# Kernel tuning notes

Hardware: AMD Instinct MI355X
Metric: run time of the kernel (lower is better)

Reference implementation:

```python
import jax, jax.numpy as jnp
import numpy as np

N = 50000      # nodes
E = 625000     # directed edges
F_IN, H1, H2, OUT = 128, 128, 64, 50


def setup_inputs() -> dict:
    key = jax.random.key(0)
    ks = jax.random.split(key, 5)
    x = jax.random.normal(ks[0], (N, F_IN), dtype=jnp.float32)
    edge_index = jax.random.randint(ks[1], (2, E), 0, N, dtype=jnp.int64)
    W1 = jax.random.normal(ks[2], (F_IN, H1), dtype=jnp.float32) * 0.05
    b1 = jnp.zeros((H1,), jnp.float32)
    W2 = jax.random.normal(ks[3], (H1, H2), dtype=jnp.float32) * 0.05
    b2 = jnp.zeros((H2,), jnp.float32)
    Wh = jax.random.normal(ks[4], (H2, OUT), dtype=jnp.float32) * 0.05
    bh = jnp.zeros((OUT,), jnp.float32)
    return {"x": x, "edge_index": edge_index, "W1": W1, "b1": b1,
            "W2": W2, "b2": b2, "Wh": Wh, "bh": bh}


def _gcn_conv(h, W, b, src, dst, dinv, n):
    # h' = D^{-1/2} A_hat D^{-1/2} (h W) + b, A_hat includes self-loops
    h = h @ W                                   # [n, out]
    coef = (dinv[src] * dinv[dst])[:, None]      # [e, 1]
    agg = jax.ops.segment_sum(h[src] * coef, dst, num_segments=n)
    return agg + b


def reference(x, edge_index, W1, b1, W2, b2, Wh, bh):
    n = x.shape[0]
    loops = jnp.arange(n, dtype=edge_index.dtype)
    src = jnp.concatenate([edge_index[0], loops])
    dst = jnp.concatenate([edge_index[1], loops])
    # symmetric GCN normalization: deg over destinations (incl. self-loops)
    deg = jax.ops.segment_sum(jnp.ones(src.shape[0], x.dtype), dst, num_segments=n)
    dinv = jnp.where(deg > 0, jax.lax.rsqrt(deg), 0.0)
    # dropout is a no-op in eval mode (training=False)
    h = _gcn_conv(x, W1, b1, src, dst, dinv, n)
    h = jax.nn.relu(h)
    h = _gcn_conv(h, W2, b2, src, dst, dinv, n)
    h = jax.nn.relu(h)
    return h @ Wh + bh
```

## Files before the change

kernel.cpp:

```cpp
#include <hip/hip_runtime.h>

#define F_IN 128
#define HH1 128
#define HH2 64
#define FOUT 50
#define EB 256
#define NBUCK_MAX 256

typedef __attribute__((ext_vector_type(8))) short short8;
typedef __attribute__((ext_vector_type(4))) short s16x4;
typedef __attribute__((ext_vector_type(4))) float f32x4;

__device__ inline short f2bf(float f) {
    union { float f; unsigned u; } v; v.f = f;
    unsigned r = v.u + 0x7fffu + ((v.u >> 16) & 1u);
    return (short)(r >> 16);
}
__device__ inline float bf2f(short s) {
    union { float f; unsigned u; } v; v.u = ((unsigned)(unsigned short)s) << 16;
    return v.f;
}

__device__ inline int detect64(const unsigned* raw) {
    __shared__ int s_is64;
    if (threadIdx.x == 0) s_is64 = 1;
    __syncthreads();
    if (raw[2 * threadIdx.x + 1] != 0u) atomicAnd(&s_is64, 0);
    __syncthreads();
    return s_is64;
}

__global__ __launch_bounds__(256) void bucket_count(
    const int* __restrict__ raw, int E, int nbuck, int* __restrict__ parthist,
    const float* __restrict__ W1, const float* __restrict__ W2,
    const float* __restrict__ Wh, short* __restrict__ W1t,
    short* __restrict__ W2t, short* __restrict__ Wht) {
    __shared__ int hist[NBUCK_MAX];
    const int tid = threadIdx.x;
    int is64 = detect64((const unsigned*)raw);
    for (int k = tid; k < nbuck; k += 256) hist[k] = 0;
    __syncthreads();
    const int CH = (E + EB - 1) / EB;
    const int e0 = blockIdx.x * CH, e1 = min(E, e0 + CH);
    for (int e = e0 + tid; e < e1; e += 256) {
        int d = is64 ? raw[2 * (long)E + 2 * e] : raw[E + e];
        atomicAdd(&hist[d >> 8], 1);
    }
    __syncthreads();
    for (int k = tid; k < nbuck; k += 256) parthist[blockIdx.x * nbuck + k] = hist[k];
    const int T1 = HH1 * F_IN, T2 = HH2 * HH1, T3 = 64 * HH2;
    int idx = blockIdx.x * 256 + tid;
    if (idx < T1) {
        int c = idx / F_IN, k = idx - c * F_IN;
        W1t[idx] = f2bf(W1[(long)k * HH1 + c]);
    } else if (idx < T1 + T2) {
        int i = idx - T1;
        int c = i / HH1, k = i - c * HH1;
        W2t[i] = f2bf(W2[(long)k * HH2 + c]);
    } else if (idx < T1 + T2 + T3) {
        int i = idx - T1 - T2;
        int c = i / HH2, k = i - c * HH2;
        Wht[i] = f2bf((c < FOUT) ? Wh[(long)k * FOUT + c] : 0.f);
    }
}

__global__ __launch_bounds__(256) void scan_cols(
    int* __restrict__ parthist, int* __restrict__ totals, int* __restrict__ bbase,
    unsigned* __restrict__ done, int nbuck, int E) {
    const int k = blockIdx.x;
    const int t = threadIdx.x;
    __shared__ int sh[256];
    int v = 0;
    if (k < nbuck) v = parthist[t * nbuck + k];
    sh[t] = v;
    __syncthreads();
    for (int off = 1; off < 256; off <<= 1) {
        int tv = (t >= off) ? sh[t - off] : 0;
        __syncthreads();
        sh[t] += tv;
        __syncthreads();
    }
    if (k < nbuck) parthist[t * nbuck + k] = sh[t] - v;
    if (t == 255) totals[k] = (k < nbuck) ? sh[255] : 0;
    __threadfence();
    __syncthreads();
    __shared__ unsigned s_old;
    if (t == 0) s_old = atomicAdd(done, 1u);
    __syncthreads();
    if (s_old % 256u != 255u) return;
    __threadfence();
    int tv2 = totals[t];
    sh[t] = tv2;
    __syncthreads();
    for (int off = 1; off < 256; off <<= 1) {
        int tt = (t >= off) ? sh[t - off] : 0;
        __syncthreads();
        sh[t] += tt;
        __syncthreads();
    }
    if (t < nbuck) bbase[t] = sh[t] - tv2;
    if (t == 0) bbase[nbuck] = E;
}

__global__ __launch_bounds__(256) void scatter_gemm1(
    const int* __restrict__ raw, int E, int nbuck,
    const int* __restrict__ parthist, const int* __restrict__ bbase,
    int2* __restrict__ tmp,
    const float* __restrict__ x, const short* __restrict__ W1t,
    short* __restrict__ h1, int n) {
    const int tid = threadIdx.x;
    if (blockIdx.x < EB) {
        __shared__ int cur[NBUCK_MAX];
        int is64 = detect64((const unsigned*)raw);
        for (int k = tid; k < nbuck; k += 256)
            cur[k] = bbase[k] + parthist[blockIdx.x * nbuck + k];
        __syncthreads();
        const int CH = (E + EB - 1) / EB;
        const int e0 = blockIdx.x * CH, e1 = min(E, e0 + CH);
        for (int e = e0 + tid; e < e1; e += 256) {
            int s, d;
            if (is64) {
                s = raw[2 * e];
                d = raw[2 * (long)E + 2 * e];
            } else {
                s = raw[e];
                d = raw[E + e];
            }
            int pos = atomicAdd(&cur[d >> 8], 1);
            tmp[pos] = make_int2(s, d);
        }
        return;
    }
    const int bid = blockIdx.x - EB;
    const int wave = tid >> 6;
    const int lane = tid & 63;
    const int l15 = lane & 15;
    const int kg = lane >> 4;
    const int rowbase = bid * 64 + wave * 16;
    const int arow = rowbase + l15;
    constexpr int KS = F_IN / 32;

    short8 af[KS];
    if (arow < n) {
        const float* xr = x + (long)arow * F_IN + kg * 8;
#pragma unroll
        for (int ks = 0; ks < KS; ++ks) {
            float4 f0 = *(const float4*)(xr + ks * 32);
            float4 f1 = *(const float4*)(xr + ks * 32 + 4);
            short8 a;
            a[0] = f2bf(f0.x); a[1] = f2bf(f0.y); a[2] = f2bf(f0.z); a[3] = f2bf(f0.w);
            a[4] = f2bf(f1.x); a[5] = f2bf(f1.y); a[6] = f2bf(f1.z); a[7] = f2bf(f1.w);
            af[ks] = a;
        }
    } else {
#pragma unroll
        for (int ks = 0; ks < KS; ++ks) af[ks] = (short8)0;
    }
    const int crowb = rowbase + kg * 4;
#pragma unroll
    for (int ct = 0; ct < HH1 / 16; ++ct) {
        const int col = ct * 16 + l15;
        const short* wr = W1t + (long)col * F_IN + kg * 8;
        f32x4 acc = {0.f, 0.f, 0.f, 0.f};
#pragma unroll
        for (int ks = 0; ks < KS; ++ks) {
            short8 bfr = *(const short8*)(wr + ks * 32);
            acc = __builtin_amdgcn_mfma_f32_16x16x32_bf16(af[ks], bfr, acc, 0, 0, 0);
        }
#pragma unroll
        for (int j = 0; j < 4; ++j) {
            int r = crowb + j;
            if (r < n) h1[(long)r * HH1 + col] = f2bf(acc[j]);
        }
    }
}

__global__ __launch_bounds__(256) void bucket_finalize(
    const int2* __restrict__ tmp, const int* __restrict__ bbase,
    int* __restrict__ rowptr, float* __restrict__ dinv,
    int* __restrict__ csr_src, int n, int nbuck) {
    __shared__ int deg[256];
    __shared__ int cur[256];
    __shared__ int sh[256];
    const int k = blockIdx.x;
    const int tid = threadIdx.x;
    const int b0 = bbase[k], b1 = bbase[k + 1];
    deg[tid] = 0;
    __syncthreads();
    for (int e = b0 + tid; e < b1; e += 256) atomicAdd(&deg[tmp[e].y & 255], 1);
    __syncthreads();
    int v = deg[tid];
    sh[tid] = v;
    __syncthreads();
    for (int off = 1; off < 256; off <<= 1) {
        int t = (tid >= off) ? sh[tid - off] : 0;
        __syncthreads();
        sh[tid] += t;
        __syncthreads();
    }
    int excl = sh[tid] - v;
    cur[tid] = excl;
    int node = (k << 8) + tid;
    if (node < n) {
        rowptr[node] = b0 + excl;
        dinv[node] = rsqrtf((float)v + 1.0f);
    }
    if (k == 0 && tid == 0) rowptr[n] = bbase[nbuck];
    __syncthreads();
    for (int e = b0 + tid; e < b1; e += 256) {
        int2 sd = tmp[e];
        int p = atomicAdd(&cur[sd.y & 255], 1);
        csr_src[b0 + p] = sd.x;
    }
}

template <int FPL>
__device__ inline void gather1(const short* p0, float c0, float* acc) {
    if constexpr (FPL == 8) {
        short8 v0 = *(const short8*)p0;
#pragma unroll
        for (int j = 0; j < 8; ++j) acc[j] = fmaf(c0, bf2f(v0[j]), acc[j]);
    } else {
        s16x4 v0 = *(const s16x4*)p0;
#pragma unroll
        for (int j = 0; j < 4; ++j) acc[j] = fmaf(c0, bf2f(v0[j]), acc[j]);
    }
}

template <int FW, bool OUT_F32>
__global__ __launch_bounds__(256) void agg_mm(
    const short* __restrict__ h, const int* __restrict__ rowptr,
    const int* __restrict__ csr_src, const float* __restrict__ dinv,
    const float* __restrict__ bias_pre, const short* __restrict__ Wt,
    const float* __restrict__ bias_post, void* __restrict__ Yv, int n,
    int ncreal) {
    constexpr int FPL = FW / 16;
    constexpr int LDW = FW + 8;
    constexpr int KS = FW / 32;
    __shared__ short tile[16][LDW];
    const int tid = threadIdx.x;
    const int grp = tid >> 4;
    const int l16 = tid & 15;
    const int node = blockIdx.x * 16 + grp;

    float acc[FPL];
#pragma unroll
    for (int j = 0; j < FPL; ++j) acc[j] = 0.f;

    if (node < n) {
        const float di = dinv[node];
#pragma unroll
        for (int j = 0; j < FPL; ++j) acc[j] = bias_pre[l16 * FPL + j];
        gather1<FPL>(h + (long)node * FW + l16 * FPL, di * di, acc);
        int e = rowptr[node];
        const int end = rowptr[node + 1];
        for (; e + 3 < end; e += 4) {
            int s0 = csr_src[e];
            int s1 = csr_src[e + 1];
            int s2 = csr_src[e + 2];
            int s3 = csr_src[e + 3];
            const short* p0 = h + (long)s0 * FW + l16 * FPL;
            const short* p1 = h + (long)s1 * FW + l16 * FPL;
            const short* p2 = h + (long)s2 * FW + l16 * FPL;
            const short* p3 = h + (long)s3 * FW + l16 * FPL;
            float c0 = dinv[s0] * di;
            float c1 = dinv[s1] * di;
            float c2 = dinv[s2] * di;
            float c3 = dinv[s3] * di;
            if constexpr (FPL == 8) {
                short8 v0 = *(const short8*)p0;
                short8 v1 = *(const short8*)p1;
                short8 v2 = *(const short8*)p2;
                short8 v3 = *(const short8*)p3;
#pragma unroll
                for (int j = 0; j < 8; ++j) acc[j] = fmaf(c0, bf2f(v0[j]), acc[j]);
#pragma unroll
                for (int j = 0; j < 8; ++j) acc[j] = fmaf(c1, bf2f(v1[j]), acc[j]);
#pragma unroll
                for (int j = 0; j < 8; ++j) acc[j] = fmaf(c2, bf2f(v2[j]), acc[j]);
#pragma unroll
                for (int j = 0; j < 8; ++j) acc[j] = fmaf(c3, bf2f(v3[j]), acc[j]);
            } else {
                s16x4 v0 = *(const s16x4*)p0;
                s16x4 v1 = *(const s16x4*)p1;
                s16x4 v2 = *(const s16x4*)p2;
                s16x4 v3 = *(const s16x4*)p3;
#pragma unroll
                for (int j = 0; j < 4; ++j) acc[j] = fmaf(c0, bf2f(v0[j]), acc[j]);
#pragma unroll
                for (int j = 0; j < 4; ++j) acc[j] = fmaf(c1, bf2f(v1[j]), acc[j]);
#pragma unroll
                for (int j = 0; j < 4; ++j) acc[j] = fmaf(c2, bf2f(v2[j]), acc[j]);
#pragma unroll
                for (int j = 0; j < 4; ++j) acc[j] = fmaf(c3, bf2f(v3[j]), acc[j]);
            }
        }
        for (; e < end; ++e) {
            int s0 = csr_src[e];
            gather1<FPL>(h + (long)s0 * FW + l16 * FPL, dinv[s0] * di, acc);
        }
    }
    if constexpr (FPL == 8) {
        short8 o;
#pragma unroll
        for (int j = 0; j < 8; ++j) o[j] = f2bf(fmaxf(acc[j], 0.f));
        *(short8*)&tile[grp][l16 * 8] = o;
    } else {
        s16x4 o;
#pragma unroll
        for (int j = 0; j < 4; ++j) o[j] = f2bf(fmaxf(acc[j], 0.f));
        *(s16x4*)&tile[grp][l16 * 4] = o;
    }
    __syncthreads();

    const int wave = tid >> 6;
    const int lane = tid & 63;
    const int l15 = lane & 15;
    const int kg = lane >> 4;
    const int col = wave * 16 + l15;
    short8 af[KS];
#pragma unroll
    for (int ks = 0; ks < KS; ++ks)
        af[ks] = *(const short8*)&tile[l15][kg * 8 + ks * 32];
    f32x4 c2 = {0.f, 0.f, 0.f, 0.f};
    const short* wr = Wt + (long)col * FW + kg * 8;
#pragma unroll
    for (int ks = 0; ks < KS; ++ks) {
        short8 bfr = *(const short8*)(wr + ks * 32);
        c2 = __builtin_amdgcn_mfma_f32_16x16x32_bf16(af[ks], bfr, c2, 0, 0, 0);
    }
    const int rb = blockIdx.x * 16 + kg * 4;
    if (OUT_F32) {
        float* Y = (float*)Yv;
#pragma unroll
        for (int j = 0; j < 4; ++j) {
            int g = rb + j;
            if (g < n && col < ncreal)
                Y[(long)g * ncreal + col] = c2[j] + bias_post[col];
        }
    } else {
        short* Y = (short*)Yv;
#pragma unroll
        for (int j = 0; j < 4; ++j) {
            int g = rb + j;
            if (g < n) Y[(long)g * 64 + col] = f2bf(c2[j]);
        }
    }
}

static inline size_t al256(size_t x) { return (x + 255) & ~(size_t)255; }

extern "C" void kernel_launch(void* const* d_in, const int* in_sizes, int n_in,
                              void* d_out, int out_size, void* d_ws, size_t ws_size,
                              hipStream_t stream) {
    const float* x    = (const float*)d_in[0];
    const int*   eraw = (const int*)d_in[1];
    const float* W1   = (const float*)d_in[2];
    const float* b1   = (const float*)d_in[3];
    const float* W2   = (const float*)d_in[4];
    const float* b2   = (const float*)d_in[5];
    const float* Wh   = (const float*)d_in[6];
    const float* bh   = (const float*)d_in[7];
    float* out = (float*)d_out;
    const int n = in_sizes[0] / F_IN;
    const int E = in_sizes[1] / 2;
    const int nbuck = (n + 255) >> 8;

    char* p = (char*)d_ws;
    unsigned* done  = (unsigned*)p; p += 256;
    float* dinv     = (float*)p; p += al256((size_t)n * 4);
    int*   rowptr   = (int*)p;   p += al256((size_t)(n + 1) * 4);
    int*   parthist = (int*)p;   p += al256((size_t)EB * nbuck * 4);
    int*   totals   = (int*)p;   p += al256((size_t)NBUCK_MAX * 4);
    int*   bbase    = (int*)p;   p += al256((size_t)(nbuck + 1) * 4);
    int*   csr_src  = (int*)p;   p += al256((size_t)E * 4);
    short* W1t      = (short*)p; p += al256((size_t)HH1 * F_IN * 2);
    short* W2t      = (short*)p; p += al256((size_t)HH2 * HH1 * 2);
    short* Whtp     = (short*)p; p += al256((size_t)64 * HH2 * 2);
    int2*  tmp      = (int2*)p;  p += al256((size_t)E * 8);
    short* h1       = (short*)p; p += al256((size_t)n * HH1 * 2);
    short* h2       = (short*)p;

    dim3 blk(256);
    bucket_count<<<EB, blk, 0, stream>>>(eraw, E, nbuck, parthist,
                                         W1, W2, Wh, W1t, W2t, Whtp);
    scan_cols<<<NBUCK_MAX, blk, 0, stream>>>(parthist, totals, bbase, done, nbuck, E);
    scatter_gemm1<<<EB + (n + 63) / 64, blk, 0, stream>>>(
        eraw, E, nbuck, parthist, bbase, tmp, x, W1t, h1, n);
    bucket_finalize<<<nbuck, blk, 0, stream>>>(tmp, bbase, rowptr, dinv, csr_src, n, nbuck);

    agg_mm<HH1, false><<<(n + 15) / 16, blk, 0, stream>>>(
        h1, rowptr, csr_src, dinv, b1, W2t, nullptr, h2, n, HH2);
    agg_mm<HH2, true><<<(n + 15) / 16, blk, 0, stream>>>(
        h2, rowptr, csr_src, dinv, b2, Whtp, bh, out, n, FOUT);
}
```

Before: 123.5 us.

## Pre-scale features by source dinv to drop per-edge dinv gathers

Folds the source-side D^{-1/2} factor into the feature rows before aggregation. h1 is scaled by a new elementwise kernel, and h2 is scaled in the first agg_mm epilogue. The gather loop then does plain adds without loading dinv[src] per edge, and the destination dinv and bias are applied once at the end. This removes random dinv loads and per-edge multiplies, at the cost of an extra read and write pass over h1 and an added rounding of the scaled values to bf16.

```diff
diff --git a/kernel.cpp b/kernel.cpp
--- a/kernel.cpp
+++ b/kernel.cpp
@@ -214,16 +214,31 @@
     }
 }
 
+__global__ __launch_bounds__(256) void scale_h1(short* __restrict__ h1,
+                                                const float* __restrict__ dinv,
+                                                int n) {
+    int idx = blockIdx.x * 256 + threadIdx.x;
+    int total = n * (HH1 / 8);
+    if (idx >= total) return;
+    int node = idx >> 4;
+    float d = dinv[node];
+    short8 v = ((const short8*)h1)[idx];
+    short8 o;
+#pragma unroll
+    for (int j = 0; j < 8; ++j) o[j] = f2bf(d * bf2f(v[j]));
+    ((short8*)h1)[idx] = o;
+}
+
 template <int FPL>
-__device__ inline void gather1(const short* p0, float c0, float* acc) {
+__device__ inline void gadd1(const short* p0, float* acc) {
     if constexpr (FPL == 8) {
         short8 v0 = *(const short8*)p0;
 #pragma unroll
-        for (int j = 0; j < 8; ++j) acc[j] = fmaf(c0, bf2f(v0[j]), acc[j]);
+        for (int j = 0; j < 8; ++j) acc[j] += bf2f(v0[j]);
     } else {
         s16x4 v0 = *(const s16x4*)p0;
 #pragma unroll
-        for (int j = 0; j < 4; ++j) acc[j] = fmaf(c0, bf2f(v0[j]), acc[j]);
+        for (int j = 0; j < 4; ++j) acc[j] += bf2f(v0[j]);
     }
 }
 
@@ -246,12 +261,11 @@
     float acc[FPL];
 #pragma unroll
     for (int j = 0; j < FPL; ++j) acc[j] = 0.f;
+    float di = 0.f;
 
     if (node < n) {
-        const float di = dinv[node];
-#pragma unroll
-        for (int j = 0; j < FPL; ++j) acc[j] = bias_pre[l16 * FPL + j];
-        gather1<FPL>(h + (long)node * FW + l16 * FPL, di * di, acc);
+        di = dinv[node];
+        gadd1<FPL>(h + (long)node * FW + l16 * FPL, acc);
         int e = rowptr[node];
         const int end = rowptr[node + 1];
         for (; e + 3 < end; e += 4) {
@@ -263,52 +277,52 @@
             const short* p1 = h + (long)s1 * FW + l16 * FPL;
             const short* p2 = h + (long)s2 * FW + l16 * FPL;
             const short* p3 = h + (long)s3 * FW + l16 * FPL;
-            float c0 = dinv[s0] * di;
-            float c1 = dinv[s1] * di;
-            float c2 = dinv[s2] * di;
-            float c3 = dinv[s3] * di;
             if constexpr (FPL == 8) {
                 short8 v0 = *(const short8*)p0;
                 short8 v1 = *(const short8*)p1;
                 short8 v2 = *(const short8*)p2;
                 short8 v3 = *(const short8*)p3;
 #pragma unroll
-                for (int j = 0; j < 8; ++j) acc[j] = fmaf(c0, bf2f(v0[j]), acc[j]);
-#pragma unroll
-                for (int j = 0; j < 8; ++j) acc[j] = fmaf(c1, bf2f(v1[j]), acc[j]);
-#pragma unroll
-                for (int j = 0; j < 8; ++j) acc[j] = fmaf(c2, bf2f(v2[j]), acc[j]);
-#pragma unroll
-                for (int j = 0; j < 8; ++j) acc[j] = fmaf(c3, bf2f(v3[j]), acc[j]);
+                for (int j = 0; j < 8; ++j) acc[j] += bf2f(v0[j]);
+#pragma unroll
+                for (int j = 0; j < 8; ++j) acc[j] += bf2f(v1[j]);
+#pragma unroll
+                for (int j = 0; j < 8; ++j) acc[j] += bf2f(v2[j]);
+#pragma unroll
+                for (int j = 0; j < 8; ++j) acc[j] += bf2f(v3[j]);
             } else {
                 s16x4 v0 = *(const s16x4*)p0;
                 s16x4 v1 = *(const s16x4*)p1;
                 s16x4 v2 = *(const s16x4*)p2;
                 s16x4 v3 = *(const s16x4*)p3;
 #pragma unroll
-                for (int j = 0; j < 4; ++j) acc[j] = fmaf(c0, bf2f(v0[j]), acc[j]);
-#pragma unroll
-                for (int j = 0; j < 4; ++j) acc[j] = fmaf(c1, bf2f(v1[j]), acc[j]);
-#pragma unroll
-                for (int j = 0; j < 4; ++j) acc[j] = fmaf(c2, bf2f(v2[j]), acc[j]);
-#pragma unroll
-                for (int j = 0; j < 4; ++j) acc[j] = fmaf(c3, bf2f(v3[j]), acc[j]);
+                for (int j = 0; j < 4; ++j) acc[j] += bf2f(v0[j]);
+#pragma unroll
+                for (int j = 0; j < 4; ++j) acc[j] += bf2f(v1[j]);
+#pragma unroll
+                for (int j = 0; j < 4; ++j) acc[j] += bf2f(v2[j]);
+#pragma unroll
+                for (int j = 0; j < 4; ++j) acc[j] += bf2f(v3[j]);
             }
         }
-        for (; e < end; ++e) {
-            int s0 = csr_src[e];
-            gather1<FPL>(h + (long)s0 * FW + l16 * FPL, dinv[s0] * di, acc);
-        }
+        for (; e < end; ++e)
+            gadd1<FPL>(h + (long)csr_src[e] * FW + l16 * FPL, acc);
     }
     if constexpr (FPL == 8) {
         short8 o;
 #pragma unroll
-        for (int j = 0; j < 8; ++j) o[j] = f2bf(fmaxf(acc[j], 0.f));
+        for (int j = 0; j < 8; ++j) {
+            float t = (node < n) ? fmaf(di, acc[j], bias_pre[l16 * 8 + j]) : 0.f;
+            o[j] = f2bf(fmaxf(t, 0.f));
+        }
         *(short8*)&tile[grp][l16 * 8] = o;
     } else {
         s16x4 o;
 #pragma unroll
-        for (int j = 0; j < 4; ++j) o[j] = f2bf(fmaxf(acc[j], 0.f));
+        for (int j = 0; j < 4; ++j) {
+            float t = (node < n) ? fmaf(di, acc[j], bias_pre[l16 * 4 + j]) : 0.f;
+            o[j] = f2bf(fmaxf(t, 0.f));
+        }
         *(s16x4*)&tile[grp][l16 * 4] = o;
     }
     __syncthreads();
@@ -343,7 +357,7 @@
 #pragma unroll
         for (int j = 0; j < 4; ++j) {
             int g = rb + j;
-            if (g < n) Y[(long)g * 64 + col] = f2bf(c2[j]);
+            if (g < n) Y[(long)g * 64 + col] = f2bf(dinv[g] * c2[j]);
         }
     }
 }
@@ -388,6 +402,7 @@
     scatter_gemm1<<<EB + (n + 63) / 64, blk, 0, stream>>>(
         eraw, E, nbuck, parthist, bbase, tmp, x, W1t, h1, n);
     bucket_finalize<<<nbuck, blk, 0, stream>>>(tmp, bbase, rowptr, dinv, csr_src, n, nbuck);
+    scale_h1<<<(n * (HH1 / 8) + 255) / 256, blk, 0, stream>>>(h1, dinv, n);
 
     agg_mm<HH1, false><<<(n + 15) / 16, blk, 0, stream>>>(
         h1, rowptr, csr_src, dinv, b1, W2t, nullptr, h2, n, HH2);
```

Result: slower. 139.7 us (+13.1%).
